# Kernel tuning notes

Measured on AMD Instinct MI355X. Metric: run time of the kernel, lower is better.

## Reference

```python
import jax, jax.numpy as jnp
import numpy as np

TAU = 20.0            # membrane time constant
TAU_ADAPT = 20.0      # threshold adaptation time constant
BETA = 1.8            # adaptation strength (n_regular=0 -> all neurons adaptive)
DAMPENING = 1.0       # surrogate-gradient dampening
REF_PERIOD = 2.0      # refractory period (steps)
THR = 0.03            # base threshold
INTERNAL_CURRENT = 0.0


@jax.custom_vjp
def spike_fn(v_sc):
    # Heaviside forward; triangular pseudo-derivative backward.
    return (v_sc > 0.0).astype(v_sc.dtype)

def _spike_fwd(v_sc):
    return spike_fn(v_sc), v_sc

def _spike_bwd(v_sc, g):
    # triangular pseudo-derivative: dampening * max(0, 1 - |v_sc|) (sharpness=1)
    return (g * DAMPENING * jnp.maximum(0.0, 1.0 - jnp.abs(v_sc)),)

spike_fn.defvjp(_spike_fwd, _spike_bwd)


def setup_inputs() -> dict:
    key = jax.random.key(0)
    kx, kin, krec = jax.random.split(key, 3)
    B, T, NI, N = 128, 500, 256, 256
    x = jax.random.normal(kx, (B, T, NI), dtype=jnp.float32)
    w_in = jax.random.normal(kin, (NI, N), dtype=jnp.float32) / np.float32(np.sqrt(NI))
    w_rec = jax.random.normal(krec, (N, N), dtype=jnp.float32) / np.float32(np.sqrt(N))
    zeros = jnp.zeros((B, N), dtype=jnp.float32)
    return {"x": x, "w_in": w_in, "w_rec": w_rec,
            "z0": zeros, "v0": zeros, "a0": zeros, "lsd0": zeros}


def _lsnn_scan(x, w_in, w_rec, z0, v0, a0, lsd0):
    n = w_rec.shape[0]
    mask = 1.0 - jnp.eye(n, dtype=x.dtype)          # zero out self-connections
    w_rec_m = mask * w_rec
    decay_v = jnp.exp(jnp.asarray(-1.0 / TAU, x.dtype))
    decay_a = jnp.exp(jnp.asarray(-1.0 / TAU_ADAPT, x.dtype))
    beta_vec = jnp.full((n,), BETA, dtype=x.dtype)  # n_regular = 0

    def step(carry, x_t):
        old_z, old_v, old_a, lsd = carry
        # currents: external + masked recurrent + constant internal
        i_in = x_t @ w_in + old_z @ w_rec_m + INTERNAL_CURRENT
        # adaptive threshold dynamics
        new_a = decay_a * old_a + (1.0 - decay_a) * old_z
        thr = THR + new_a * beta_vec
        # voltage dynamics with reset current
        i_reset = -thr * old_z
        new_v = decay_v * old_v + (1.0 - decay_v) * i_in + i_reset
        # surrogate spike
        v_sc = (new_v - thr) / thr
        z = spike_fn(v_sc)
        # refractoriness
        non_ref = (lsd >= REF_PERIOD).astype(x.dtype)
        z = non_ref * z
        new_lsd = (lsd + 1.0) * (1.0 - z)
        return (z, new_v, new_a, new_lsd), (z, new_v, thr, v_sc)

    x_t_first = jnp.swapaxes(x, 0, 1)               # [T, B, n_in]
    _, (zs, vs, thrs, vscs) = jax.lax.scan(step, (z0, v0, a0, lsd0), x_t_first)
    # stack the 4 per-step outputs -> [4, T, B, N]
    return jnp.stack([zs, vs, thrs, vscs], axis=0)


def reference(x, w_in, w_rec, z0, v0, a0, lsd0):
    return _lsnn_scan(x, w_in, w_rec, z0, v0, a0, lsd0)
```

## Files before the change

kernel.cpp:

```cpp
#include <hip/hip_runtime.h>

#define T_STEPS 500
#define N_NEUR  256
#define N_IN    256
#define N_BATCH 128

__global__ __launch_bounds__(256) void xw_gemm_kernel(
    const float* __restrict__ A,
    const float* __restrict__ W,
    float* __restrict__ C)
{
    __shared__ float As[16][129];
    __shared__ float Bs[16][68];
    const int tid = threadIdx.x;
    const int bm  = blockIdx.x;
    const int bn  = blockIdx.y;
    const int ty  = tid >> 4;
    const int tx  = tid & 15;
    const int arow  = tid >> 1;
    const int akoff = (tid & 1) * 8;
    const int brow  = tid >> 4;
    const int bcol  = (tid & 15) * 4;
    const float* Ab = A + (size_t)bm * 128 * 256;

    float acc[8][4];
#pragma unroll
    for (int i = 0; i < 8; ++i)
#pragma unroll
        for (int j = 0; j < 4; ++j) acc[i][j] = 0.f;

    for (int k0 = 0; k0 < 256; k0 += 16) {
        float4 av0 = *(const float4*)(Ab + (size_t)arow * 256 + k0 + akoff);
        float4 av1 = *(const float4*)(Ab + (size_t)arow * 256 + k0 + akoff + 4);
        float4 bv  = *(const float4*)(W + (size_t)(k0 + brow) * 256 + bn * 64 + bcol);
        __syncthreads();
        As[akoff + 0][arow] = av0.x; As[akoff + 1][arow] = av0.y;
        As[akoff + 2][arow] = av0.z; As[akoff + 3][arow] = av0.w;
        As[akoff + 4][arow] = av1.x; As[akoff + 5][arow] = av1.y;
        As[akoff + 6][arow] = av1.z; As[akoff + 7][arow] = av1.w;
        *(float4*)&Bs[brow][bcol] = bv;
        __syncthreads();
#pragma unroll
        for (int kk = 0; kk < 16; ++kk) {
            float a[8], b[4];
#pragma unroll
            for (int i = 0; i < 8; ++i) a[i] = As[kk][ty * 8 + i];
#pragma unroll
            for (int j = 0; j < 4; ++j) b[j] = Bs[kk][tx * 4 + j];
#pragma unroll
            for (int i = 0; i < 8; ++i)
#pragma unroll
                for (int j = 0; j < 4; ++j)
                    acc[i][j] += a[i] * b[j];
        }
    }
    const int crow = bm * 128 + ty * 8;
    const int ccol = bn * 64 + tx * 4;
#pragma unroll
    for (int i = 0; i < 8; ++i) {
        float4 v = make_float4(acc[i][0], acc[i][1], acc[i][2], acc[i][3]);
        *(float4*)(C + (size_t)(crow + i) * 256 + ccol) = v;
    }
}

__global__ void prep_wrec_kernel(const float* __restrict__ w_rec,
                                 float* __restrict__ wz)
{
    int i = blockIdx.x * 256 + threadIdx.x;
    if (i < 256 * 256) {
        int r = i >> 8, c = i & 255;
        wz[i] = (r == c) ? 0.f : w_rec[i];
    } else {
        wz[i] = 0.f;
    }
}

__device__ __forceinline__ unsigned long long rfl64(unsigned long long q) {
    unsigned hi = (unsigned)__builtin_amdgcn_readfirstlane((int)(q >> 32));
    unsigned lo = (unsigned)__builtin_amdgcn_readfirstlane((int)(unsigned)q);
    return ((unsigned long long)hi << 32) | (unsigned long long)lo;
}

__global__ __launch_bounds__(256) void lsnn_scan2_kernel(
    const float* __restrict__ xw,
    const float* __restrict__ wz,
    const float* __restrict__ z0, const float* __restrict__ v0,
    const float* __restrict__ a0, const float* __restrict__ lsd0,
    float* __restrict__ out)
{
    const int b    = blockIdx.x;
    const int n    = threadIdx.x;
    const int lane = n & 63;
    const int wid  = n >> 6;

    __shared__ unsigned long long msk[2][4];

    const float dv   = (float)0.9512294245007140018;
    const float omdv = 1.0f - dv;

    const int bn = b * N_NEUR + n;
    float z   = z0[bn];
    float v   = v0[bn];
    float a   = a0[bn];
    float lsd = lsd0[bn];

    {
        unsigned long long wm = __ballot(z != 0.f);
        if (lane == 0) msk[0][wid] = wm;
    }
    __syncthreads();

    float x_next = xw[((size_t)b * T_STEPS) * N_NEUR + n];
    const size_t PL = (size_t)T_STEPS * N_BATCH * N_NEUR;

    for (int t = 0; t < T_STEPS; ++t) {
        float x_cur = x_next;
        {
            int tn = (t + 1 < T_STEPS) ? t + 1 : t;
            x_next = xw[((size_t)b * T_STEPS + tn) * N_NEUR + n];
        }

        const int rb = t & 1;
        unsigned long long m0 = rfl64(msk[rb][0]);
        unsigned long long m1 = rfl64(msk[rb][1]);
        unsigned long long m2 = rfl64(msk[rb][2]);
        unsigned long long m3 = rfl64(msk[rb][3]);

        const int c0 = __popcll(m0), c1 = __popcll(m1);
        const int c2 = __popcll(m2), c3 = __popcll(m3);
        const int mx = max(max(c0, c1), max(c2, c3));

        float p0 = 0.f, p1 = 0.f, p2 = 0.f, p3 = 0.f;
        for (int i0 = 0; i0 < mx; i0 += 8) {
            int id0[8], id1[8], id2[8], id3[8];
#pragma unroll
            for (int j = 0; j < 8; ++j) {
                id0[j] = m0 ? (__builtin_ctzll(m0) + 0)   : 256;  m0 &= m0 - 1;
                id1[j] = m1 ? (__builtin_ctzll(m1) + 64)  : 256;  m1 &= m1 - 1;
                id2[j] = m2 ? (__builtin_ctzll(m2) + 128) : 256;  m2 &= m2 - 1;
                id3[j] = m3 ? (__builtin_ctzll(m3) + 192) : 256;  m3 &= m3 - 1;
            }
            float w0[8], w1[8], w2[8], w3[8];
#pragma unroll
            for (int j = 0; j < 8; ++j) {
                w0[j] = wz[id0[j] * N_NEUR + n];
                w1[j] = wz[id1[j] * N_NEUR + n];
                w2[j] = wz[id2[j] * N_NEUR + n];
                w3[j] = wz[id3[j] * N_NEUR + n];
            }
#pragma unroll
            for (int j = 0; j < 8; ++j) {
                p0 += w0[j]; p1 += w1[j]; p2 += w2[j]; p3 += w3[j];
            }
        }
        float i_rec = ((p0 + p1) + p2) + p3;

        float i_in  = x_cur + i_rec;
        float new_a = dv * a + omdv * z;
        float thr   = 0.03f + new_a * 1.8f;
        float new_v = dv * v + omdv * i_in - thr * z;
        float v_sc  = (new_v - thr) / thr;
        float zs    = (v_sc > 0.f) ? 1.f : 0.f;
        zs          = (lsd >= 2.0f) ? zs : 0.f;
        float new_lsd = (lsd + 1.f) * (1.f - zs);

        size_t o = (size_t)t * (N_BATCH * N_NEUR) + (size_t)b * N_NEUR + n;
        __builtin_nontemporal_store(zs,    out + o);
        __builtin_nontemporal_store(new_v, out + o + PL);
        __builtin_nontemporal_store(thr,   out + o + 2 * PL);
        __builtin_nontemporal_store(v_sc,  out + o + 3 * PL);

        v = new_v; a = new_a; lsd = new_lsd; z = zs;

        {
            unsigned long long wm = __ballot(zs != 0.f);
            if (lane == 0) msk[rb ^ 1][wid] = wm;
        }
        __syncthreads();
    }
}

template <bool USE_XW>
__global__ __launch_bounds__(256) void lsnn_scan_kernel(
    const float* __restrict__ xin,
    const float* __restrict__ w_in,
    const float* __restrict__ w_rec,
    const float* __restrict__ z0, const float* __restrict__ v0,
    const float* __restrict__ a0, const float* __restrict__ lsd0,
    float* __restrict__ out)
{
    const int b    = blockIdx.x;
    const int n    = threadIdx.x;
    const int lane = n & 63;
    const int wid  = n >> 6;

    __shared__ int   cnt4[4];
    __shared__ int   act[256];
    __shared__ float xsh[256];

    const float dv   = (float)0.9512294245007140018;
    const float omdv = 1.0f - dv;

    const int base_bn = b * N_NEUR + n;
    float z   = z0[base_bn];
    float v   = v0[base_bn];
    float a   = a0[base_bn];
    float lsd = lsd0[base_bn];

    act[n] = 0;
    {
        unsigned long long wm = __ballot(z != 0.f);
        if (lane == 0) cnt4[wid] = __popcll(wm);
        if (z != 0.f) {
            int pos = __popcll(wm & ((1ull << lane) - 1ull));
            act[wid * 64 + pos] = n;
        }
        if (!USE_XW) xsh[n] = xin[((size_t)b * T_STEPS) * N_IN + n];
    }
    __syncthreads();

    float x_next = USE_XW ? xin[((size_t)b * T_STEPS) * N_NEUR + n] : 0.f;

    for (int t = 0; t < T_STEPS; ++t) {
        float x_cur = x_next;
        if (USE_XW) {
            int tn = (t + 1 < T_STEPS) ? t + 1 : t;
            x_next = xin[((size_t)b * T_STEPS + tn) * N_NEUR + n];
        }
        const int cs0 = cnt4[0], cs1 = cnt4[1], cs2 = cnt4[2], cs3 = cnt4[3];
        int mx = max(max(cs0, cs1), max(cs2, cs3));
        float r0 = 0.f, r1 = 0.f, r2 = 0.f, r3 = 0.f;
        for (int i0 = 0; i0 < mx; i0 += 8) {
            float wv[4][8];
            bool  ok[4][8];
#pragma unroll
            for (int s = 0; s < 4; ++s) {
                const int cs = (s == 0) ? cs0 : (s == 1) ? cs1 : (s == 2) ? cs2 : cs3;
#pragma unroll
                for (int j = 0; j < 8; ++j) {
                    int ii = i0 + j;
                    int m  = act[s * 64 + (ii < cs ? ii : 0)] & 255;
                    wv[s][j] = w_rec[m * N_NEUR + n];
                    ok[s][j] = (ii < cs) && (m != n);
                }
            }
#pragma unroll
            for (int j = 0; j < 8; ++j) r0 += ok[0][j] ? wv[0][j] : 0.f;
#pragma unroll
            for (int j = 0; j < 8; ++j) r1 += ok[1][j] ? wv[1][j] : 0.f;
#pragma unroll
            for (int j = 0; j < 8; ++j) r2 += ok[2][j] ? wv[2][j] : 0.f;
#pragma unroll
            for (int j = 0; j < 8; ++j) r3 += ok[3][j] ? wv[3][j] : 0.f;
        }
        float i_rec = ((r0 + r1) + r2) + r3;

        float xdot;
        if (USE_XW) {
            xdot = x_cur;
        } else {
            float s = 0.f;
#pragma unroll 8
            for (int m = 0; m < N_IN; ++m) s += xsh[m] * w_in[m * N_NEUR + n];
            xdot = s;
        }
        float i_in = xdot + i_rec;

        float new_a = dv * a + omdv * z;
        float thr   = 0.03f + new_a * 1.8f;
        float new_v = dv * v + omdv * i_in - thr * z;
        float v_sc  = (new_v - thr) / thr;
        float zs    = (v_sc > 0.f) ? 1.f : 0.f;
        zs          = (lsd >= 2.0f) ? zs : 0.f;
        float new_lsd = (lsd + 1.f) * (1.f - zs);

        const size_t PL = (size_t)T_STEPS * N_BATCH * N_NEUR;
        size_t o = (size_t)t * (N_BATCH * N_NEUR) + (size_t)b * N_NEUR + n;
        out[o]          = zs;
        out[o + PL]     = new_v;
        out[o + 2 * PL] = thr;
        out[o + 3 * PL] = v_sc;

        v = new_v; a = new_a; lsd = new_lsd; z = zs;

        __syncthreads();
        unsigned long long wm = __ballot(zs != 0.f);
        if (lane == 0) cnt4[wid] = __popcll(wm);
        if (zs != 0.f) {
            int pos = __popcll(wm & ((1ull << lane) - 1ull));
            act[wid * 64 + pos] = n;
        }
        if (!USE_XW && (t + 1 < T_STEPS))
            xsh[n] = xin[((size_t)b * T_STEPS + t + 1) * N_IN + n];
        __syncthreads();
    }
}

extern "C" void kernel_launch(void* const* d_in, const int* in_sizes, int n_in,
                              void* d_out, int out_size, void* d_ws, size_t ws_size,
                              hipStream_t stream) {
    const float* x     = (const float*)d_in[0];
    const float* w_in  = (const float*)d_in[1];
    const float* w_rec = (const float*)d_in[2];
    const float* z0    = (const float*)d_in[3];
    const float* v0    = (const float*)d_in[4];
    const float* a0    = (const float*)d_in[5];
    const float* lsd0  = (const float*)d_in[6];
    float* out = (float*)d_out;

    const size_t xw_bytes = (size_t)N_BATCH * T_STEPS * N_NEUR * sizeof(float);
    const size_t wz_bytes = (size_t)257 * 256 * sizeof(float);

    if (ws_size >= xw_bytes + wz_bytes) {
        float* xw = (float*)d_ws;
        float* wz = (float*)((char*)d_ws + xw_bytes);
        prep_wrec_kernel<<<257, 256, 0, stream>>>(w_rec, wz);
        dim3 grid(500, 4, 1);
        xw_gemm_kernel<<<grid, 256, 0, stream>>>(x, w_in, xw);
        lsnn_scan2_kernel<<<N_BATCH, 256, 0, stream>>>(
            xw, wz, z0, v0, a0, lsd0, out);
    } else if (ws_size >= xw_bytes) {
        float* xw = (float*)d_ws;
        dim3 grid(500, 4, 1);
        xw_gemm_kernel<<<grid, 256, 0, stream>>>(x, w_in, xw);
        lsnn_scan_kernel<true><<<N_BATCH, 256, 0, stream>>>(
            xw, nullptr, w_rec, z0, v0, a0, lsd0, out);
    } else {
        lsnn_scan_kernel<false><<<N_BATCH, 256, 0, stream>>>(
            x, w_in, w_rec, z0, v0, a0, lsd0, out);
    }
}
```

Before: 897.8 us.

## Widen GEMM tiles with register prefetch; deepen xw prefetch and lighten scan barrier

The input-projection GEMM now computes 128x128 tiles (8x8 per thread) instead of 128x64. It prefetches the next K-slice of global data into registers while the current slice is being computed, and pads the shared B tile to avoid bank conflicts. The scan kernel prefetches the projected input two steps ahead instead of one. It also replaces __syncthreads with an explicit lgkmcnt wait plus s_barrier, so the loop does not wait on outstanding global loads and stores. The larger GEMM tile raises register pressure, and the scan, which is latency-bound over 500 steps on only 128 blocks, probably dominates total time.

After: 1.217 ms. +35.6%, slower.

```diff
diff --git a/kernel.cpp b/kernel.cpp
--- a/kernel.cpp
+++ b/kernel.cpp
@@ -5,13 +5,15 @@
 #define N_IN    256
 #define N_BATCH 128
 
-__global__ __launch_bounds__(256) void xw_gemm_kernel(
+#define BPOS(c) ((c) + (((c) >> 4) << 2))
+
+__global__ __launch_bounds__(256, 4) void xw_gemm3_kernel(
     const float* __restrict__ A,
     const float* __restrict__ W,
     float* __restrict__ C)
 {
-    __shared__ float As[16][129];
-    __shared__ float Bs[16][68];
+    __shared__ float As[16][132];
+    __shared__ float Bs[16][160];
     const int tid = threadIdx.x;
     const int bm  = blockIdx.x;
     const int bn  = blockIdx.y;
@@ -20,46 +22,57 @@
     const int arow  = tid >> 1;
     const int akoff = (tid & 1) * 8;
     const int brow  = tid >> 4;
-    const int bcol  = (tid & 15) * 4;
+    const int bcol  = (tid & 15) * 8;
     const float* Ab = A + (size_t)bm * 128 * 256;
 
-    float acc[8][4];
+    float acc[8][8];
 #pragma unroll
     for (int i = 0; i < 8; ++i)
 #pragma unroll
-        for (int j = 0; j < 4; ++j) acc[i][j] = 0.f;
+        for (int j = 0; j < 8; ++j) acc[i][j] = 0.f;
+
+    float4 av0 = *(const float4*)(Ab + (size_t)arow * 256 + akoff);
+    float4 av1 = *(const float4*)(Ab + (size_t)arow * 256 + akoff + 4);
+    float4 bv0 = *(const float4*)(W + (size_t)brow * 256 + bn * 128 + bcol);
+    float4 bv1 = *(const float4*)(W + (size_t)brow * 256 + bn * 128 + bcol + 4);
 
     for (int k0 = 0; k0 < 256; k0 += 16) {
-        float4 av0 = *(const float4*)(Ab + (size_t)arow * 256 + k0 + akoff);
-        float4 av1 = *(const float4*)(Ab + (size_t)arow * 256 + k0 + akoff + 4);
-        float4 bv  = *(const float4*)(W + (size_t)(k0 + brow) * 256 + bn * 64 + bcol);
         __syncthreads();
         As[akoff + 0][arow] = av0.x; As[akoff + 1][arow] = av0.y;
         As[akoff + 2][arow] = av0.z; As[akoff + 3][arow] = av0.w;
         As[akoff + 4][arow] = av1.x; As[akoff + 5][arow] = av1.y;
         As[akoff + 6][arow] = av1.z; As[akoff + 7][arow] = av1.w;
-        *(float4*)&Bs[brow][bcol] = bv;
+        *(float4*)&Bs[brow][BPOS(bcol)]     = bv0;
+        *(float4*)&Bs[brow][BPOS(bcol) + 4] = bv1;
         __syncthreads();
+        if (k0 + 16 < 256) {
+            av0 = *(const float4*)(Ab + (size_t)arow * 256 + k0 + 16 + akoff);
+            av1 = *(const float4*)(Ab + (size_t)arow * 256 + k0 + 16 + akoff + 4);
+            bv0 = *(const float4*)(W + (size_t)(k0 + 16 + brow) * 256 + bn * 128 + bcol);
+            bv1 = *(const float4*)(W + (size_t)(k0 + 16 + brow) * 256 + bn * 128 + bcol + 4);
+        }
 #pragma unroll
         for (int kk = 0; kk < 16; ++kk) {
-            float a[8], b[4];
+            float a[8], b[8];
 #pragma unroll
             for (int i = 0; i < 8; ++i) a[i] = As[kk][ty * 8 + i];
 #pragma unroll
-            for (int j = 0; j < 4; ++j) b[j] = Bs[kk][tx * 4 + j];
+            for (int j = 0; j < 8; ++j) b[j] = Bs[kk][BPOS(tx * 8) + j];
 #pragma unroll
             for (int i = 0; i < 8; ++i)
 #pragma unroll
-                for (int j = 0; j < 4; ++j)
+                for (int j = 0; j < 8; ++j)
                     acc[i][j] += a[i] * b[j];
         }
     }
     const int crow = bm * 128 + ty * 8;
-    const int ccol = bn * 64 + tx * 4;
+    const int ccol = bn * 128 + tx * 8;
 #pragma unroll
     for (int i = 0; i < 8; ++i) {
-        float4 v = make_float4(acc[i][0], acc[i][1], acc[i][2], acc[i][3]);
-        *(float4*)(C + (size_t)(crow + i) * 256 + ccol) = v;
+        float4 v0 = make_float4(acc[i][0], acc[i][1], acc[i][2], acc[i][3]);
+        float4 v1 = make_float4(acc[i][4], acc[i][5], acc[i][6], acc[i][7]);
+        *(float4*)(C + (size_t)(crow + i) * 256 + ccol)     = v0;
+        *(float4*)(C + (size_t)(crow + i) * 256 + ccol + 4) = v1;
     }
 }
 
@@ -81,7 +94,7 @@
     return ((unsigned long long)hi << 32) | (unsigned long long)lo;
 }
 
-__global__ __launch_bounds__(256) void lsnn_scan2_kernel(
+__global__ __launch_bounds__(256) void lsnn_scan6_kernel(
     const float* __restrict__ xw,
     const float* __restrict__ wz,
     const float* __restrict__ z0, const float* __restrict__ v0,
@@ -93,7 +106,7 @@
     const int lane = n & 63;
     const int wid  = n >> 6;
 
-    __shared__ unsigned long long msk[2][4];
+    __shared__ __align__(16) unsigned long long msk[2][4];
 
     const float dv   = (float)0.9512294245007140018;
     const float omdv = 1.0f - dv;
@@ -110,14 +123,16 @@
     }
     __syncthreads();
 
-    float x_next = xw[((size_t)b * T_STEPS) * N_NEUR + n];
+    float x1 = xw[((size_t)b * T_STEPS) * N_NEUR + n];
+    float x2 = xw[((size_t)b * T_STEPS + (T_STEPS > 1 ? 1 : 0)) * N_NEUR + n];
     const size_t PL = (size_t)T_STEPS * N_BATCH * N_NEUR;
 
     for (int t = 0; t < T_STEPS; ++t) {
-        float x_cur = x_next;
+        float x_cur = x1;
+        x1 = x2;
         {
-            int tn = (t + 1 < T_STEPS) ? t + 1 : t;
-            x_next = xw[((size_t)b * T_STEPS + tn) * N_NEUR + n];
+            int tn = (t + 2 < T_STEPS) ? t + 2 : T_STEPS - 1;
+            x2 = xw[((size_t)b * T_STEPS + tn) * N_NEUR + n];
         }
 
         const int rb = t & 1;
@@ -176,7 +191,9 @@
             unsigned long long wm = __ballot(zs != 0.f);
             if (lane == 0) msk[rb ^ 1][wid] = wm;
         }
-        __syncthreads();
+        asm volatile("s_waitcnt lgkmcnt(0)" ::: "memory");
+        __builtin_amdgcn_s_barrier();
+        asm volatile("" ::: "memory");
     }
 }
 
@@ -234,14 +251,14 @@
             float wv[4][8];
             bool  ok[4][8];
 #pragma unroll
-            for (int s = 0; s < 4; ++s) {
-                const int cs = (s == 0) ? cs0 : (s == 1) ? cs1 : (s == 2) ? cs2 : cs3;
+            for (int sgi = 0; sgi < 4; ++sgi) {
+                const int cs = (sgi == 0) ? cs0 : (sgi == 1) ? cs1 : (sgi == 2) ? cs2 : cs3;
 #pragma unroll
                 for (int j = 0; j < 8; ++j) {
                     int ii = i0 + j;
-                    int m  = act[s * 64 + (ii < cs ? ii : 0)] & 255;
-                    wv[s][j] = w_rec[m * N_NEUR + n];
-                    ok[s][j] = (ii < cs) && (m != n);
+                    int m  = act[sgi * 64 + (ii < cs ? ii : 0)] & 255;
+                    wv[sgi][j] = w_rec[m * N_NEUR + n];
+                    ok[sgi][j] = (ii < cs) && (m != n);
                 }
             }
 #pragma unroll
@@ -259,10 +276,10 @@
         if (USE_XW) {
             xdot = x_cur;
         } else {
-            float s = 0.f;
+            float sum = 0.f;
 #pragma unroll 8
-            for (int m = 0; m < N_IN; ++m) s += xsh[m] * w_in[m * N_NEUR + n];
-            xdot = s;
+            for (int m = 0; m < N_IN; ++m) sum += xsh[m] * w_in[m * N_NEUR + n];
+            xdot = sum;
         }
         float i_in = xdot + i_rec;
 
@@ -315,14 +332,14 @@
         float* xw = (float*)d_ws;
         float* wz = (float*)((char*)d_ws + xw_bytes);
         prep_wrec_kernel<<<257, 256, 0, stream>>>(w_rec, wz);
-        dim3 grid(500, 4, 1);
-        xw_gemm_kernel<<<grid, 256, 0, stream>>>(x, w_in, xw);
-        lsnn_scan2_kernel<<<N_BATCH, 256, 0, stream>>>(
+        dim3 grid(500, 2, 1);
+        xw_gemm3_kernel<<<grid, 256, 0, stream>>>(x, w_in, xw);
+        lsnn_scan6_kernel<<<N_BATCH, 256, 0, stream>>>(
             xw, wz, z0, v0, a0, lsd0, out);
     } else if (ws_size >= xw_bytes) {
         float* xw = (float*)d_ws;
-        dim3 grid(500, 4, 1);
-        xw_gemm_kernel<<<grid, 256, 0, stream>>>(x, w_in, xw);
+        dim3 grid(500, 2, 1);
+        xw_gemm3_kernel<<<grid, 256, 0, stream>>>(x, w_in, xw);
         lsnn_scan_kernel<true><<<N_BATCH, 256, 0, stream>>>(
             xw, nullptr, w_rec, z0, v0, a0, lsd0, out);
     } else {
```
